# Optimization experiments

Hardware: AMD Instinct MI355X
Metric: run time of the kernel (lower is better)

Reference implementation:

```python
import jax, jax.numpy as jnp
import numpy as np

NUM_HEADS = 12

def setup_inputs() -> dict:
    key = jax.random.key(0)
    k1, k2, k3, k4 = jax.random.split(key, 4)
    B, T, N, C = 8, 16, 196, 768
    x = jax.random.normal(k1, (B, T, N, C), dtype=jnp.float32)
    # qkv Linear (no bias): stored as [C, 3C] so y = x @ W_qkv
    W_qkv = jax.random.normal(k2, (C, 3 * C), dtype=jnp.float32) * (C ** -0.5)
    W_proj = jax.random.normal(k3, (C, C), dtype=jnp.float32) * (C ** -0.5)
    b_proj = jax.random.normal(k4, (C,), dtype=jnp.float32) * 0.02
    return {"x": x, "W_qkv": W_qkv, "W_proj": W_proj, "b_proj": b_proj}

def reference(x, W_qkv, W_proj, b_proj):
    B, T, N, C = x.shape
    H = NUM_HEADS
    hd = C // H
    scale = hd ** -0.5
    # shared QKV projection -> [3, B, T, H, N, hd]
    qkv = (x @ W_qkv).reshape(B, T, N, 3, H, hd).transpose(3, 0, 1, 4, 2, 5)
    q, k, v = qkv[0], qkv[1], qkv[2]
    # spatial attention over N (per frame)
    attn = jax.nn.softmax(jnp.einsum('bthnd,bthmd->bthnm', q, k) * scale, axis=-1)
    x1 = jnp.einsum('bthnm,bthmd->bthnd', attn, v)
    x1 = x1.transpose(0, 1, 3, 2, 4).reshape(B, T, N, C)  # [B,T,N,H,hd]->[B,T,N,C]
    # temporal attention over T (per spatial token): permute to [B,H,N,T,hd]
    q2 = q.transpose(0, 2, 3, 1, 4)
    k2 = k.transpose(0, 2, 3, 1, 4)
    v2 = v.transpose(0, 2, 3, 1, 4)
    attn2 = jax.nn.softmax(jnp.einsum('bhntd,bhnsd->bhnts', q2, k2) * scale, axis=-1)
    x2 = jnp.einsum('bhnts,bhnsd->bhntd', attn2, v2)
    x2 = x2.transpose(0, 3, 2, 1, 4).reshape(B, T, N, C)  # [B,T,N,H,hd]->[B,T,N,C]
    # average the two branches, then output projection
    return ((x1 + x2) * 0.5) @ W_proj + b_proj
```

## Files before the change

### kernel.cpp

```cpp
#include <hip/hip_runtime.h>
#include <cstdint>
#include <cstddef>

typedef unsigned short ushort_t;
typedef unsigned int   uint_t;

#define B_   8
#define T_   16
#define N_   196
#define C_   768
#define H_   12
#define C3_  2304
#define M_   25088

#define NP_  208
#define KS_  72
#define VS_  232
#define PS_  232

#define TS_  40

typedef __attribute__((ext_vector_type(8))) short short8;
typedef __attribute__((ext_vector_type(4))) float floatx4;

__device__ __forceinline__ float bf2f(ushort_t u) {
  return __uint_as_float(((uint_t)u) << 16);
}
__device__ __forceinline__ ushort_t f2bf(float f) {
  uint_t u = __float_as_uint(f);
  u += 0x7FFFu + ((u >> 16) & 1u);
  return (ushort_t)(u >> 16);
}
__device__ __forceinline__ uint_t pack2(float a, float b) {
  return (uint_t)f2bf(a) | ((uint_t)f2bf(b) << 16);
}

__device__ __forceinline__ void gload_lds16(const ushort_t* g, ushort_t* l) {
  __builtin_amdgcn_global_load_lds(
      (const __attribute__((address_space(1))) uint_t*)g,
      (__attribute__((address_space(3))) uint_t*)l, 16, 0, 0);
}

__global__ void fsta_prep(const float* __restrict__ x,
                          ushort_t* __restrict__ xbf,
                          const float* __restrict__ Wqkv,
                          ushort_t* __restrict__ WtQkv,
                          const float* __restrict__ Wproj,
                          ushort_t* __restrict__ WtProj)
{
  const int bid = blockIdx.x;
  const int tid = threadIdx.x;
  if (bid < 9408) {
    int i = (bid * 256 + tid) * 8;
    const float* f = x + i;
    uint4 u;
    u.x = pack2(f[0], f[1]); u.y = pack2(f[2], f[3]);
    u.z = pack2(f[4], f[5]); u.w = pack2(f[6], f[7]);
    *(uint4*)(xbf + i) = u;
  } else if (bid < 16320) {
    int o = (bid - 9408) * 256 + tid;
    int c = o / 768;
    int r = o - c * 768;
    WtQkv[o] = f2bf(Wqkv[(size_t)r * 2304 + c]);
  } else {
    int o = (bid - 16320) * 256 + tid;
    int c = o / 768;
    int r = o - c * 768;
    WtProj[o] = f2bf(Wproj[(size_t)r * 768 + c]);
  }
}

template <typename OutT>
__global__ __launch_bounds__(256) void fsta_gemm_bt(
    const ushort_t* __restrict__ A1,
    const ushort_t* __restrict__ Bt,
    const float* __restrict__ bias,
    OutT* __restrict__ Cout,
    int Ncols, int K)
{
  __shared__ ushort_t As[128 * 32];
  __shared__ ushort_t Bs[128 * 32];
  const int tid  = threadIdx.x;

  const int nbx = gridDim.x;
  const int nwg = nbx * gridDim.y;
  int lin = blockIdx.y * nbx + blockIdx.x;
  if ((nwg & 7) == 0) {
    const int cpx = nwg >> 3;
    lin = (lin & 7) * cpx + (lin >> 3);
  }
  const int m0 = (lin % nbx) * 128;
  const int n0 = (lin / nbx) * 128;

  const int lane = tid & 63;
  const int wv   = tid >> 6;
  const int wr   = (wv >> 1) * 64;
  const int wc   = (wv & 1) * 64;
  const int lrow = lane & 15;
  const int k8   = (lane >> 4) * 8;

  const int srow = lane >> 2;
  const int scol = (lane & 3) * 8;

  floatx4 acc[4][4];
#pragma unroll
  for (int i = 0; i < 4; ++i)
#pragma unroll
    for (int j = 0; j < 4; ++j)
      acc[i][j] = (floatx4){0.f, 0.f, 0.f, 0.f};

  for (int k0 = 0; k0 < K; k0 += 32) {
#pragma unroll
    for (int i = 0; i < 2; ++i) {
      const int ch = wv * 2 + i;
      const ushort_t* ga =
          A1 + (size_t)(m0 + ch * 16 + srow) * K + k0 + scol;
      gload_lds16(ga, &As[ch * 512]);
      const ushort_t* gb =
          Bt + (size_t)(n0 + ch * 16 + srow) * K + k0 + scol;
      gload_lds16(gb, &Bs[ch * 512]);
    }
    __syncthreads();

    short8 af[4], bfr[4];
#pragma unroll
    for (int i = 0; i < 4; ++i)
      af[i] = *(const short8*)&As[(wr + i * 16 + lrow) * 32 + k8];
#pragma unroll
    for (int i = 0; i < 4; ++i)
      bfr[i] = *(const short8*)&Bs[(wc + i * 16 + lrow) * 32 + k8];

#pragma unroll
    for (int i = 0; i < 4; ++i)
#pragma unroll
      for (int j = 0; j < 4; ++j)
        acc[i][j] = __builtin_amdgcn_mfma_f32_16x16x32_bf16(
            af[i], bfr[j], acc[i][j], 0, 0, 0);
    __syncthreads();
  }

  const int qd = lane >> 4;
#pragma unroll
  for (int i = 0; i < 4; ++i) {
    int row = m0 + wr + i * 16 + qd * 4;
#pragma unroll
    for (int j = 0; j < 4; ++j) {
      int col = n0 + wc + j * 16 + lrow;
      float badd = bias ? bias[col] : 0.f;
#pragma unroll
      for (int r = 0; r < 4; ++r) {
        float v = acc[i][j][r] + badd;
        if constexpr (sizeof(OutT) == 4)
          Cout[(size_t)(row + r) * Ncols + col] = v;
        else
          Cout[(size_t)(row + r) * Ncols + col] = (OutT)f2bf(v);
      }
    }
  }
}

__global__ __launch_bounds__(512) void fsta_spatial(
    const ushort_t* __restrict__ qkv, ushort_t* __restrict__ x1)
{
  __shared__ ushort_t Ks[NP_ * KS_];
  __shared__ ushort_t Vt[64 * VS_];
  __shared__ ushort_t Ps[8][16 * PS_];
  const int tid = threadIdx.x;
  const int bid = blockIdx.x;
  const int h   = bid % H_;
  const int bt  = bid / H_;
  const size_t rowbase = (size_t)bt * N_ * C3_;
  const int hofs = h * 64;

  for (int idx = tid; idx < N_ * 8; idx += 512) {
    int n = idx >> 3, c = (idx & 7) * 8;
    size_t so = rowbase + (size_t)n * C3_ + hofs + c;
    *(uint4*)&Ks[n * KS_ + c] = *(const uint4*)(qkv + so + 768);
    uint4 v = *(const uint4*)(qkv + so + 1536);
    ushort_t tmp[8];
    *(uint4*)tmp = v;
#pragma unroll
    for (int i = 0; i < 8; ++i) Vt[(c + i) * VS_ + n] = tmp[i];
  }
  for (int idx = tid; idx < 64 * (VS_ - N_); idx += 512) {
    int d = idx / (VS_ - N_), k = N_ + idx % (VS_ - N_);
    Vt[d * VS_ + k] = 0;
  }
  __syncthreads();

  const int lane = tid & 63;
  const int wv   = tid >> 6;
  const int lrow = lane & 15;
  const int quad = lane >> 4;
  const int k8   = quad * 8;

  for (int qt = wv; qt < 13; qt += 8) {
    int qrow = qt * 16 + lrow; if (qrow > N_ - 1) qrow = N_ - 1;
    const ushort_t* qp = qkv + rowbase + (size_t)qrow * C3_ + hofs;
    short8 qf0 = *(const short8*)(qp + k8);
    short8 qf1 = *(const short8*)(qp + 32 + k8);

    floatx4 s[13];
#pragma unroll
    for (int kt = 0; kt < 13; ++kt) {
      const ushort_t* kp = &Ks[(kt * 16 + lrow) * KS_];
      short8 kf0 = *(const short8*)(kp + k8);
      short8 kf1 = *(const short8*)(kp + 32 + k8);
      floatx4 a = (floatx4){0.f, 0.f, 0.f, 0.f};
      a = __builtin_amdgcn_mfma_f32_16x16x32_bf16(qf0, kf0, a, 0, 0, 0);
      a = __builtin_amdgcn_mfma_f32_16x16x32_bf16(qf1, kf1, a, 0, 0, 0);
      s[kt] = a;
    }

    if (lrow >= 4)
      s[12] = (floatx4){-INFINITY, -INFINITY, -INFINITY, -INFINITY};

    float mx[4], sum[4];
#pragma unroll
    for (int r = 0; r < 4; ++r) {
      float m2 = s[0][r];
#pragma unroll
      for (int kt = 1; kt < 13; ++kt) m2 = fmaxf(m2, s[kt][r]);
#pragma unroll
      for (int xm = 1; xm < 16; xm <<= 1) m2 = fmaxf(m2, __shfl_xor(m2, xm, 64));
      mx[r] = m2;
    }
#pragma unroll
    for (int r = 0; r < 4; ++r) {
      float sm = 0.f;
#pragma unroll
      for (int kt = 0; kt < 13; ++kt) {
        float p = __expf((s[kt][r] - mx[r]) * 0.125f);
        s[kt][r] = p;
        sm += p;
      }
#pragma unroll
      for (int xm = 1; xm < 16; xm <<= 1) sm += __shfl_xor(sm, xm, 64);
      sum[r] = sm;
    }

    ushort_t* pw = Ps[wv];
#pragma unroll
    for (int kt = 0; kt < 13; ++kt)
#pragma unroll
      for (int r = 0; r < 4; ++r)
        pw[(quad * 4 + r) * PS_ + kt * 16 + lrow] = f2bf(s[kt][r]);
#pragma unroll
    for (int r = 0; r < 4; ++r)
      pw[(quad * 4 + r) * PS_ + 208 + lrow] = 0;

    floatx4 o[4];
#pragma unroll
    for (int nt = 0; nt < 4; ++nt) o[nt] = (floatx4){0.f, 0.f, 0.f, 0.f};
#pragma unroll
    for (int kt = 0; kt < 7; ++kt) {
      short8 pf = *(const short8*)&pw[lrow * PS_ + kt * 32 + k8];
#pragma unroll
      for (int nt = 0; nt < 4; ++nt) {
        short8 vf = *(const short8*)&Vt[(nt * 16 + lrow) * VS_ + kt * 32 + k8];
        o[nt] = __builtin_amdgcn_mfma_f32_16x16x32_bf16(pf, vf, o[nt], 0, 0, 0);
      }
    }

    float inv[4];
#pragma unroll
    for (int r = 0; r < 4; ++r) inv[r] = 1.f / sum[r];
#pragma unroll
    for (int nt = 0; nt < 4; ++nt) {
#pragma unroll
      for (int r = 0; r < 4; ++r) {
        int qr = qt * 16 + quad * 4 + r;
        if (qr < N_)
          x1[(size_t)(bt * N_ + qr) * C_ + hofs + nt * 16 + lrow] =
              f2bf(o[nt][r] * inv[r]);
      }
    }
  }
}

__global__ __launch_bounds__(256) void fsta_temporal(
    const ushort_t* __restrict__ qkv, ushort_t* __restrict__ xavg)
{
  __shared__ ushort_t Pt[4][16 * TS_];
  __shared__ ushort_t Vw[4][64 * TS_];
  const int tid  = threadIdx.x;
  const int lane = tid & 63;
  const int wv   = tid >> 6;
  const int gw   = blockIdx.x * 4 + wv;
  const int n    = gw % N_;
  const int bh   = gw / N_;
  const int h    = bh % H_;
  const int b    = bh / H_;
  const int hofs = h * 64;
  const int lrow = lane & 15;
  const int quad = lane >> 4;
  const int k8   = quad * 8;

  ushort_t* pw = Pt[wv];
  ushort_t* vw = Vw[wv];

  for (int i = lane; i < 16 * 16; i += 64)
    pw[(i >> 4) * TS_ + 16 + (i & 15)] = 0;
  for (int i = lane; i < 64 * 16; i += 64)
    vw[(i >> 4) * TS_ + 16 + (i & 15)] = 0;

  for (int i = lane; i < 128; i += 64) {
    int s = i >> 3, c8 = (i & 7) * 8;
    size_t vo = ((size_t)((b * T_ + s) * N_ + n)) * C3_ + hofs + 1536 + c8;
    ushort_t tmp[8];
    *(uint4*)tmp = *(const uint4*)(qkv + vo);
#pragma unroll
    for (int j = 0; j < 8; ++j) vw[(c8 + j) * TS_ + s] = tmp[j];
  }

  const size_t ro = ((size_t)((b * T_ + lrow) * N_ + n)) * C3_ + hofs;
  short8 qf0 = *(const short8*)(qkv + ro + k8);
  short8 qf1 = *(const short8*)(qkv + ro + 32 + k8);
  short8 kf0 = *(const short8*)(qkv + ro + 768 + k8);
  short8 kf1 = *(const short8*)(qkv + ro + 800 + k8);

  floatx4 s4 = (floatx4){0.f, 0.f, 0.f, 0.f};
  s4 = __builtin_amdgcn_mfma_f32_16x16x32_bf16(qf0, kf0, s4, 0, 0, 0);
  s4 = __builtin_amdgcn_mfma_f32_16x16x32_bf16(qf1, kf1, s4, 0, 0, 0);

  float inv[4];
#pragma unroll
  for (int r = 0; r < 4; ++r) {
    float m2 = s4[r];
#pragma unroll
    for (int xm = 1; xm < 16; xm <<= 1) m2 = fmaxf(m2, __shfl_xor(m2, xm, 64));
    float p = __expf((s4[r] - m2) * 0.125f);
    float sm = p;
#pragma unroll
    for (int xm = 1; xm < 16; xm <<= 1) sm += __shfl_xor(sm, xm, 64);
    pw[(quad * 4 + r) * TS_ + lrow] = f2bf(p);
    inv[r] = 1.f / sm;
  }

  short8 pf = *(const short8*)&pw[lrow * TS_ + k8];
  floatx4 o[4];
#pragma unroll
  for (int nt = 0; nt < 4; ++nt) {
    short8 vf = *(const short8*)&vw[(nt * 16 + lrow) * TS_ + k8];
    o[nt] = __builtin_amdgcn_mfma_f32_16x16x32_bf16(
        pf, vf, (floatx4){0.f, 0.f, 0.f, 0.f}, 0, 0, 0);
  }

#pragma unroll
  for (int nt = 0; nt < 4; ++nt)
#pragma unroll
    for (int r = 0; r < 4; ++r) {
      int t = quad * 4 + r;
      size_t xo = ((size_t)((b * T_ + t) * N_ + n)) * C_ + hofs + nt * 16 + lrow;
      float prev = bf2f(xavg[xo]);
      xavg[xo] = f2bf(0.5f * (prev + o[nt][r] * inv[r]));
    }
}

extern "C" void kernel_launch(void* const* d_in, const int* in_sizes, int n_in,
                              void* d_out, int out_size, void* d_ws, size_t ws_size,
                              hipStream_t stream)
{
  (void)in_sizes; (void)n_in; (void)out_size; (void)ws_size;
  const float* x     = (const float*)d_in[0];
  const float* Wqkv  = (const float*)d_in[1];
  const float* Wproj = (const float*)d_in[2];
  const float* bproj = (const float*)d_in[3];
  float*    out = (float*)d_out;
  ushort_t* ws  = (ushort_t*)d_ws;

  ushort_t* WtQkv  = ws;
  ushort_t* WtProj = ws + 1769472;
  ushort_t* xbf    = ws + 2359296;
  ushort_t* xavg   = xbf;
  ushort_t* qkv    = ws + 21626880;

  fsta_prep<<<dim3(18624), dim3(256), 0, stream>>>(
      x, xbf, Wqkv, WtQkv, Wproj, WtProj);
  fsta_gemm_bt<ushort_t><<<dim3(196, 18), dim3(256), 0, stream>>>(
      xbf, WtQkv, (const float*)nullptr, qkv, 2304, 768);
  fsta_spatial<<<dim3(B_ * T_ * H_), dim3(512), 0, stream>>>(qkv, xavg);
  fsta_temporal<<<dim3((B_ * H_ * N_) / 4), dim3(256), 0, stream>>>(qkv, xavg);
  fsta_gemm_bt<float><<<dim3(196, 6), dim3(256), 0, stream>>>(
      xavg, WtProj, bproj, out, 768, 768);
}
```

Before: 446.1 us.

## Replace GEMM with 256x256 tiled, double-buffered, swizzled-LDS pipelined kernel

Replaces the 128x128 single-buffered bf16 GEMM with a 256x256 tile kernel using 8 waves, a K-step of 64 and double-buffered LDS staging. Global-to-LDS loads for the next stage are interleaved with MFMA phases under explicit vmcnt waits and barriers. The LDS layout gets an XOR swizzle to avoid bank conflicts, and the workgroup-to-XCD remap now handles grid sizes that are not a multiple of 8. The aim is higher data reuse per tile and overlap of memory loads with compute. The trade-offs are 128KB of LDS and a large accumulator array, which limit occupancy, and the proj GEMM now launches only 294 workgroups.

New measurement: 426.9 us. -4.3%, faster.

```diff
diff --git a/kernel.cpp b/kernel.cpp
--- a/kernel.cpp
+++ b/kernel.cpp
@@ -39,6 +39,12 @@
   __builtin_amdgcn_global_load_lds(
       (const __attribute__((address_space(1))) uint_t*)g,
       (__attribute__((address_space(3))) uint_t*)l, 16, 0, 0);
+}
+
+__device__ __forceinline__ void bar() {
+  asm volatile("" ::: "memory");
+  __builtin_amdgcn_s_barrier();
+  __builtin_amdgcn_sched_barrier(0);
 }
 
 __global__ void fsta_prep(const float* __restrict__ x,
@@ -70,90 +76,125 @@
   }
 }
 
+#define STG(X, rb, bu, xo, kss, t)                                            \
+  { _Pragma("unroll") for (int c_ = 0; c_ < 2; ++c_) {                        \
+      const ushort_t* g_ = (X) +                                              \
+          (size_t)((rb) + c_ * 128 + wv * 16 + srow) * K +                    \
+          (t) * 64 + (kss) * 32 + chnk * 8;                                   \
+      gload_lds16(g_, &lds[(bu) * 32768 + (xo) + (kss) * 8192 +               \
+                           c_ * 4096 + wv * 512]); } }
+
+#define PH(bu, mh, kss, DOB, GUARD, ...)                                      \
+  { short8 af[4];                                                             \
+    _Pragma("unroll") for (int m2 = 0; m2 < 4; ++m2) {                        \
+      int rr = wm * 128 + ((mh) * 4 + m2) * 16 + lrow;                        \
+      af[m2] = *(const short8*)&lds[(bu) * 32768 + (kss) * 8192 +             \
+                                    rr * 32 + rch8]; }                        \
+    if (DOB) {                                                                \
+      _Pragma("unroll") for (int n2 = 0; n2 < 4; ++n2) {                      \
+        int rr = wn * 64 + n2 * 16 + lrow;                                    \
+        bf[n2] = *(const short8*)&lds[(bu) * 32768 + 16384 + (kss) * 8192 +   \
+                                      rr * 32 + rch8]; } }                    \
+    __VA_ARGS__                                                               \
+    GUARD                                                                     \
+    bar();                                                                    \
+    __builtin_amdgcn_s_setprio(1);                                            \
+    _Pragma("unroll") for (int m2 = 0; m2 < 4; ++m2)                          \
+      _Pragma("unroll") for (int n2 = 0; n2 < 4; ++n2)                        \
+        acc[(mh) * 4 + m2][n2] = __builtin_amdgcn_mfma_f32_16x16x32_bf16(     \
+            af[m2], bf[n2], acc[(mh) * 4 + m2][n2], 0, 0, 0);                 \
+    __builtin_amdgcn_s_setprio(0);                                            \
+    bar(); }
+
+#define GUARD_NONE
+#define GUARD4 asm volatile("s_waitcnt vmcnt(4)" ::: "memory");
+#define GUARD0 asm volatile("s_waitcnt vmcnt(0)" ::: "memory");
+
 template <typename OutT>
-__global__ __launch_bounds__(256) void fsta_gemm_bt(
+__global__ __launch_bounds__(512) void fsta_gemm256(
     const ushort_t* __restrict__ A1,
     const ushort_t* __restrict__ Bt,
     const float* __restrict__ bias,
     OutT* __restrict__ Cout,
     int Ncols, int K)
 {
-  __shared__ ushort_t As[128 * 32];
-  __shared__ ushort_t Bs[128 * 32];
+  __shared__ ushort_t lds[65536];
   const int tid  = threadIdx.x;
-
-  const int nbx = gridDim.x;
-  const int nwg = nbx * gridDim.y;
-  int lin = blockIdx.y * nbx + blockIdx.x;
-  if ((nwg & 7) == 0) {
-    const int cpx = nwg >> 3;
-    lin = (lin & 7) * cpx + (lin >> 3);
-  }
-  const int m0 = (lin % nbx) * 128;
-  const int n0 = (lin / nbx) * 128;
-
   const int lane = tid & 63;
   const int wv   = tid >> 6;
-  const int wr   = (wv >> 1) * 64;
-  const int wc   = (wv & 1) * 64;
+  const int wm   = wv >> 2;
+  const int wn   = wv & 3;
   const int lrow = lane & 15;
-  const int k8   = (lane >> 4) * 8;
-
+  const int quad = lane >> 4;
+  const int rch8 = (quad ^ (lrow & 3)) * 8;
   const int srow = lane >> 2;
-  const int scol = (lane & 3) * 8;
-
-  floatx4 acc[4][4];
-#pragma unroll
-  for (int i = 0; i < 4; ++i)
+  const int chnk = (lane & 3) ^ (srow & 3);
+
+  const int ntx = gridDim.x;
+  const int nwg = ntx * gridDim.y;
+  int lin = blockIdx.y * ntx + blockIdx.x;
+  {
+    int q = nwg >> 3, r = nwg & 7;
+    int xcd = lin & 7, off = lin >> 3;
+    lin = (xcd < r ? xcd * (q + 1) : r * (q + 1) + (xcd - r) * q) + off;
+  }
+  const int m0 = (lin % ntx) * 256;
+  const int n0 = (lin / ntx) * 256;
+
+  const int NT = K >> 6;
+  const int NI = NT >> 1;
+
+  floatx4 acc[8][4];
+#pragma unroll
+  for (int i = 0; i < 8; ++i)
 #pragma unroll
     for (int j = 0; j < 4; ++j)
       acc[i][j] = (floatx4){0.f, 0.f, 0.f, 0.f};
 
-  for (int k0 = 0; k0 < K; k0 += 32) {
-#pragma unroll
-    for (int i = 0; i < 2; ++i) {
-      const int ch = wv * 2 + i;
-      const ushort_t* ga =
-          A1 + (size_t)(m0 + ch * 16 + srow) * K + k0 + scol;
-      gload_lds16(ga, &As[ch * 512]);
-      const ushort_t* gb =
-          Bt + (size_t)(n0 + ch * 16 + srow) * K + k0 + scol;
-      gload_lds16(gb, &Bs[ch * 512]);
-    }
-    __syncthreads();
-
-    short8 af[4], bfr[4];
-#pragma unroll
-    for (int i = 0; i < 4; ++i)
-      af[i] = *(const short8*)&As[(wr + i * 16 + lrow) * 32 + k8];
-#pragma unroll
-    for (int i = 0; i < 4; ++i)
-      bfr[i] = *(const short8*)&Bs[(wc + i * 16 + lrow) * 32 + k8];
-
-#pragma unroll
-    for (int i = 0; i < 4; ++i)
-#pragma unroll
-      for (int j = 0; j < 4; ++j)
-        acc[i][j] = __builtin_amdgcn_mfma_f32_16x16x32_bf16(
-            af[i], bfr[j], acc[i][j], 0, 0, 0);
-    __syncthreads();
-  }
-
-  const int qd = lane >> 4;
-#pragma unroll
-  for (int i = 0; i < 4; ++i) {
-    int row = m0 + wr + i * 16 + qd * 4;
-#pragma unroll
-    for (int j = 0; j < 4; ++j) {
-      int col = n0 + wc + j * 16 + lrow;
+  STG(A1, m0, 0, 0,     0, 0)
+  STG(Bt, n0, 0, 16384, 0, 0)
+  STG(A1, m0, 0, 0,     1, 0)
+  STG(Bt, n0, 0, 16384, 1, 0)
+  STG(A1, m0, 1, 0,     0, 1)
+  STG(Bt, n0, 1, 16384, 0, 1)
+  GUARD4
+  bar();
+
+  short8 bf[4];
+  for (int i = 0; i < NI; ++i) {
+    const int t0 = 2 * i;
+    const bool lastI = (i == NI - 1);
+    PH(0, 0, 0, 1, GUARD_NONE,
+       { STG(A1, m0, 1, 0, 1, t0 + 1) STG(Bt, n0, 1, 16384, 1, t0 + 1) })
+    PH(0, 1, 0, 0, GUARD_NONE, )
+    PH(0, 0, 1, 1, GUARD_NONE,
+       { if (!lastI) { STG(A1, m0, 0, 0, 0, t0 + 2) } })
+    PH(0, 1, 1, 0, if (lastI) { GUARD0 } else { GUARD4 },
+       { if (!lastI) { STG(Bt, n0, 0, 16384, 0, t0 + 2) } })
+    PH(1, 0, 0, 1, GUARD_NONE,
+       { if (!lastI) { STG(A1, m0, 0, 0, 1, t0 + 2)
+                       STG(Bt, n0, 0, 16384, 1, t0 + 2) } })
+    PH(1, 1, 0, 0, GUARD_NONE, )
+    PH(1, 0, 1, 1, GUARD_NONE,
+       { if (!lastI) { STG(A1, m0, 1, 0, 0, t0 + 3) } })
+    PH(1, 1, 1, 0, if (!lastI) { GUARD4 },
+       { if (!lastI) { STG(Bt, n0, 1, 16384, 0, t0 + 3) } })
+  }
+
+#pragma unroll
+  for (int m2 = 0; m2 < 8; ++m2) {
+    int row = m0 + wm * 128 + m2 * 16 + quad * 4;
+#pragma unroll
+    for (int n2 = 0; n2 < 4; ++n2) {
+      int col = n0 + wn * 64 + n2 * 16 + lrow;
       float badd = bias ? bias[col] : 0.f;
 #pragma unroll
-      for (int r = 0; r < 4; ++r) {
-        float v = acc[i][j][r] + badd;
+      for (int rr = 0; rr < 4; ++rr) {
+        float v = acc[m2][n2][rr] + badd;
         if constexpr (sizeof(OutT) == 4)
-          Cout[(size_t)(row + r) * Ncols + col] = v;
+          Cout[(size_t)(row + rr) * Ncols + col] = v;
         else
-          Cout[(size_t)(row + r) * Ncols + col] = (OutT)f2bf(v);
+          Cout[(size_t)(row + rr) * Ncols + col] = (OutT)f2bf(v);
       }
     }
   }
@@ -377,10 +418,10 @@
 
   fsta_prep<<<dim3(18624), dim3(256), 0, stream>>>(
       x, xbf, Wqkv, WtQkv, Wproj, WtProj);
-  fsta_gemm_bt<ushort_t><<<dim3(196, 18), dim3(256), 0, stream>>>(
+  fsta_gemm256<ushort_t><<<dim3(98, 9), dim3(512), 0, stream>>>(
       xbf, WtQkv, (const float*)nullptr, qkv, 2304, 768);
   fsta_spatial<<<dim3(B_ * T_ * H_), dim3(512), 0, stream>>>(qkv, xavg);
   fsta_temporal<<<dim3((B_ * H_ * N_) / 4), dim3(256), 0, stream>>>(qkv, xavg);
-  fsta_gemm_bt<float><<<dim3(196, 6), dim3(256), 0, stream>>>(
+  fsta_gemm256<float><<<dim3(98, 3), dim3(512), 0, stream>>>(
       xavg, WtProj, bproj, out, 768, 768);
 }
```
